# Performance work log

Hardware: AMD Instinct MI355X
Metric: run time of the kernel (lower is better)

## Reference

```python
import jax, jax.numpy as jnp
import numpy as np

N_NODES = 50000
N_EDGES = 1200000
IN_DIM = 256
OUT_DIM = 64
SLOPE = 0.2


def setup_inputs() -> dict:
    key = jax.random.key(0)
    k1, k2, k3, k4, k5 = jax.random.split(key, 5)
    h = jax.random.normal(k1, (N_NODES, IN_DIM), dtype=jnp.float32)
    # xavier_normal-ish scale for the linear weights
    W_fc = jax.random.normal(k2, (OUT_DIM, IN_DIM), dtype=jnp.float32) * (2.0 / (IN_DIM + OUT_DIM)) ** 0.5
    W_attn = jax.random.normal(k3, (1, 2 * OUT_DIM), dtype=jnp.float32) * (2.0 / (2 * OUT_DIM + 1)) ** 0.5
    src = jax.random.randint(k4, (N_EDGES,), 0, N_NODES, dtype=jnp.int32)
    dst = jax.random.randint(k5, (N_EDGES,), 0, N_NODES, dtype=jnp.int32)
    return {"h": h, "W_fc": W_fc, "W_attn": W_attn, "src": src, "dst": dst}


def reference(h, W_fc, W_attn, src, dst):
    # node transform: z = fc(h)                      [N, D]
    z = h @ W_fc.T
    # split attn weight so we never materialize the [E, 2D] concat
    a = W_attn[0]
    a_src, a_dst = a[:OUT_DIM], a[OUT_DIM:]
    s_src = z @ a_src            # [N]
    s_dst = z @ a_dst            # [N]
    # per-edge score: leaky_relu(attn_fc([z_src, z_dst]))
    e = jax.nn.leaky_relu(s_src[src] + s_dst[dst], negative_slope=SLOPE)  # [E]
    # edge softmax over incoming edges of each dst node
    m = jax.ops.segment_max(e, dst, num_segments=N_NODES)                 # [N]
    ex = jnp.exp(e - m[dst])                                              # [E]
    denom = jax.ops.segment_sum(ex, dst, num_segments=N_NODES)            # [N]
    alpha = ex / denom[dst]                                               # [E]
    # weighted scatter-sum of source features, then ELU
    agg = jax.ops.segment_sum(alpha[:, None] * z[src], dst, num_segments=N_NODES)  # [N, D]
    return jax.nn.elu(agg)
```

## Files before the change

### kernel.cpp

```cpp
#include <hip/hip_runtime.h>
#include <math.h>

#define N_NODES 50000
#define N_EDGES 1200000
#define IN_DIM  256
#define OUT_DIM 64
#define SLOPE   0.2f
#define BNODES  64
#define NBKT    782
#define NBKT_PAD 1024
#define EPB     1024
#define NCHUNK  1172
#define BCAP    2048
#define SSTRIDE 2240

typedef unsigned int   uint;
typedef unsigned short ushort;
typedef float  f32x4  __attribute__((ext_vector_type(4)));
typedef short  short8 __attribute__((ext_vector_type(8)));

__device__ inline ushort bf16_rne(float f) {
    uint u = __float_as_uint(f);
    u += 0x7FFF + ((u >> 16) & 1);
    return (ushort)(u >> 16);
}
__device__ inline float bf16_f32(ushort s) {
    return __uint_as_float(((uint)s) << 16);
}
__device__ inline ushort f32_f16(float f) {
    _Float16 h = (_Float16)f;
    return __builtin_bit_cast(ushort, h);
}
__device__ inline float f16_f32(ushort u) {
    return (float)__builtin_bit_cast(_Float16, u);
}

__global__ __launch_bounds__(256) void k_binprep(const int* __restrict__ src,
                                                 const int* __restrict__ dst,
                                                 const float* __restrict__ Wfc,
                                                 ushort* __restrict__ Whi,
                                                 ushort* __restrict__ Wlo,
                                                 uint* __restrict__ binned,
                                                 uint* __restrict__ tab) {
    if (blockIdx.x >= NCHUNK) {
        int i = (blockIdx.x - NCHUNK) * 256 + threadIdx.x;
        float f = Wfc[i];
        ushort hi = bf16_rne(f);
        Whi[i] = hi;
        Wlo[i] = bf16_rne(f - bf16_f32(hi));
        return;
    }
    __shared__ uint staged[EPB];
    __shared__ int lhist[NBKT_PAD];
    __shared__ int lcur[NBKT_PAD];
    __shared__ int ws[256];
    const int t = threadIdx.x;
    const int c = blockIdx.x;
    const int base = c * EPB;
    const int n = min(EPB, N_EDGES - base);

    ((int4*)lhist)[t] = int4{0, 0, 0, 0};
    __syncthreads();

    int4 d4, s4;
    bool act = (4 * t < n);
    if (act) {
        d4 = ((const int4*)(dst + base))[t];
        s4 = ((const int4*)(src + base))[t];
        atomicAdd(&lhist[d4.x >> 6], 1);
        atomicAdd(&lhist[d4.y >> 6], 1);
        atomicAdd(&lhist[d4.z >> 6], 1);
        atomicAdd(&lhist[d4.w >> 6], 1);
    }
    __syncthreads();

    int4 hv = ((const int4*)lhist)[t];
    int lsum = hv.x + hv.y + hv.z + hv.w;
    ws[t] = lsum; __syncthreads();
    #pragma unroll
    for (int off = 1; off < 256; off <<= 1) {
        int x = (t >= off) ? ws[t - off] : 0;
        __syncthreads(); ws[t] += x; __syncthreads();
    }
    int excl = ws[t] - lsum;
    int p0 = excl, p1 = p0 + hv.x, p2 = p1 + hv.y, p3 = p2 + hv.z;
    lcur[4 * t]     = p0;
    lcur[4 * t + 1] = p1;
    lcur[4 * t + 2] = p2;
    lcur[4 * t + 3] = p3;
    uint4 te;
    te.x = ((uint)p0 << 11) | (uint)hv.x;
    te.y = ((uint)p1 << 11) | (uint)hv.y;
    te.z = ((uint)p2 << 11) | (uint)hv.z;
    te.w = ((uint)p3 << 11) | (uint)hv.w;
    ((uint4*)(tab + (size_t)c * NBKT_PAD))[t] = te;
    __syncthreads();

    if (act) {
        int dd[4] = {d4.x, d4.y, d4.z, d4.w};
        int ss[4] = {s4.x, s4.y, s4.z, s4.w};
        #pragma unroll
        for (int u = 0; u < 4; ++u) {
            int b = dd[u] >> 6, dl = dd[u] & 63;
            int slot = atomicAdd(&lcur[b], 1);
            staged[slot] = ((uint)dl << 16) | (uint)ss[u];
        }
    }
    __syncthreads();
    #pragma unroll
    for (int k = 0; k < EPB / 256; ++k) {
        int i = k * 256 + t;
        if (i < n) binned[base + i] = staged[i];
    }
}

__global__ __launch_bounds__(64) void k_gemm(const float* __restrict__ h,
                                             const ushort* __restrict__ Whi,
                                             const ushort* __restrict__ Wlo,
                                             const float* __restrict__ Wattn,
                                             ushort* __restrict__ zh,
                                             float* __restrict__ sS,
                                             float* __restrict__ sD) {
    const int l   = threadIdx.x;
    const int r16 = l & 15;
    const int g   = l >> 4;
    const int base = blockIdx.x * 16;

    const float*  ha = h   + (size_t)(base + r16) * IN_DIM + g * 8;
    const ushort* wh = Whi + (size_t)r16 * IN_DIM + g * 8;
    const ushort* wl = Wlo + (size_t)r16 * IN_DIM + g * 8;

    f32x4 c[4] = {{0,0,0,0},{0,0,0,0},{0,0,0,0},{0,0,0,0}};

    #pragma unroll
    for (int ks = 0; ks < 8; ++ks) {
        float4 a0 = *(const float4*)(ha + ks * 32);
        float4 a1 = *(const float4*)(ha + ks * 32 + 4);
        float af[8] = {a0.x, a0.y, a0.z, a0.w, a1.x, a1.y, a1.z, a1.w};
        short8 ahi;
        #pragma unroll
        for (int i = 0; i < 8; ++i) ahi[i] = (short)bf16_rne(af[i]);
        #pragma unroll
        for (int n = 0; n < 4; ++n) {
            short8 bh = *(const short8*)(wh + n * 16 * IN_DIM + ks * 32);
            short8 bl = *(const short8*)(wl + n * 16 * IN_DIM + ks * 32);
            c[n] = __builtin_amdgcn_mfma_f32_16x16x32_bf16(ahi, bh, c[n], 0, 0, 0);
            c[n] = __builtin_amdgcn_mfma_f32_16x16x32_bf16(ahi, bl, c[n], 0, 0, 0);
        }
    }

    float aSv[4], aDv[4];
    #pragma unroll
    for (int n = 0; n < 4; ++n) {
        aSv[n] = Wattn[n * 16 + r16];
        aDv[n] = Wattn[OUT_DIM + n * 16 + r16];
    }
    #pragma unroll
    for (int r = 0; r < 4; ++r) {
        int node = base + g * 4 + r;
        float ss = 0.f, sd = 0.f;
        #pragma unroll
        for (int n = 0; n < 4; ++n) {
            float v = c[n][r];
            zh[(size_t)node * OUT_DIM + n * 16 + r16] = f32_f16(v);
            ss += v * aSv[n];
            sd += v * aDv[n];
        }
        ss += __shfl_xor(ss, 1); ss += __shfl_xor(ss, 2);
        ss += __shfl_xor(ss, 4); ss += __shfl_xor(ss, 8);
        sd += __shfl_xor(sd, 1); sd += __shfl_xor(sd, 2);
        sd += __shfl_xor(sd, 4); sd += __shfl_xor(sd, 8);
        if (r16 == 0) { sS[node] = ss; sD[node] = sd; }
    }
}

__global__ __launch_bounds__(256) void k_sort(const uint* __restrict__ binned,
                                              const uint* __restrict__ tab,
                                              const float* __restrict__ sS,
                                              const float* __restrict__ sD,
                                              uint* __restrict__ srcEx,
                                              int* __restrict__ rowptrFine,
                                              int* __restrict__ cntArr) {
    __shared__ uint lstage[BCAP];
    __shared__ uint lEdge[SSTRIDE];
    __shared__ int lhist[64], lcur[64], ws[256];
    __shared__ float ldsD[64];
    __shared__ int sPtot;
    const int b = blockIdx.x, t = threadIdx.x;
    const int node = (b << 6) + t;
    if (t < 64) {
        lhist[t] = 0;
        ldsD[t] = (node < N_NODES) ? sD[node] : 0.f;
    }
    __syncthreads();

    uint runs[5];
    int nck = 0, myCnt = 0;
    for (int c = t; c < NCHUNK; c += 256) {
        uint e = tab[(size_t)c * NBKT_PAD + b];
        runs[nck++] = e;
        myCnt += (int)(e & 0x7FF);
    }
    ws[t] = myCnt; __syncthreads();
    #pragma unroll
    for (int off = 1; off < 256; off <<= 1) {
        int x = (t >= off) ? ws[t - off] : 0;
        __syncthreads(); ws[t] += x; __syncthreads();
    }
    int pos = ws[t] - myCnt;
    int n = ws[255];
    __syncthreads();

    {
        int k = 0;
        for (int c = t; c < NCHUNK; c += 256, ++k) {
            uint e = runs[k];
            int cnt = (int)(e & 0x7FF);
            const uint* pB = binned + (size_t)c * EPB + (e >> 11);
            for (int i = 0; i < cnt; ++i) {
                uint w = pB[i];
                lstage[pos++] = w;
                atomicAdd(&lhist[w >> 16], 1);
            }
        }
    }
    __syncthreads();

    int pc = 0;
    if (t < 64) { pc = (lhist[t] + 3) & ~3; ws[t] = pc; }
    __syncthreads();
    #pragma unroll
    for (int off = 1; off < 64; off <<= 1) {
        int x = 0;
        if (t < 64 && t >= off) x = ws[t - off];
        __syncthreads();
        if (t < 64) ws[t] += x;
        __syncthreads();
    }
    if (t < 64) {
        int pexcl = ws[t] - pc;
        lcur[t] = pexcl;
        for (int j = lhist[t]; j < pc; ++j) lEdge[pexcl + j] = 0;
        if (node < N_NODES) {
            rowptrFine[node] = b * SSTRIDE + pexcl;
            cntArr[node] = pc;
        }
        if (t == 63) sPtot = ws[63];
    }
    __syncthreads();

    for (int i = t; i < n; i += 256) {
        uint w = lstage[i];
        int dl = (int)(w >> 16);
        int s  = (int)(w & 0xFFFF);
        float e = sS[s] + ldsD[dl];
        e = e > 0.f ? e : SLOPE * e;
        ushort exb = f32_f16(__expf(e));
        int slot = atomicAdd(&lcur[dl], 1);
        lEdge[slot] = ((w & 0xFFFFu) << 16) | (uint)exb;
    }
    __syncthreads();

    int ptot = sPtot;
    uint* dstp = srcEx + (size_t)b * SSTRIDE;
    for (int i = t; i < ptot; i += 256) dstp[i] = lEdge[i];
}

__global__ __launch_bounds__(256) void k_aggc(const uint2* __restrict__ zrow,
                                              const uint* __restrict__ srcEx,
                                              const int* __restrict__ rowptr,
                                              const int* __restrict__ cntArr,
                                              float* __restrict__ out) {
    int node = blockIdx.x * 4 + (threadIdx.x >> 6);
    int lane = threadIdx.x & 63;
    int q = lane >> 4, ql = lane & 15;
    int beg = rowptr[node];
    int cnt4 = cntArr[node];
    float a0 = 0.f, a1 = 0.f, a2 = 0.f, a3 = 0.f, den = 0.f;
    #pragma unroll 4
    for (int i = 0; i < cnt4; i += 4) {
        uint w = srcEx[beg + i + q];
        uint2 zp = zrow[((w >> 16) << 4) + ql];
        float ex = f16_f32((ushort)(w & 0xFFFF));
        a0 += ex * f16_f32((ushort)(zp.x & 0xFFFF));
        a1 += ex * f16_f32((ushort)(zp.x >> 16));
        a2 += ex * f16_f32((ushort)(zp.y & 0xFFFF));
        a3 += ex * f16_f32((ushort)(zp.y >> 16));
        den += ex;
    }
    a0 += __shfl_xor(a0, 16); a0 += __shfl_xor(a0, 32);
    a1 += __shfl_xor(a1, 16); a1 += __shfl_xor(a1, 32);
    a2 += __shfl_xor(a2, 16); a2 += __shfl_xor(a2, 32);
    a3 += __shfl_xor(a3, 16); a3 += __shfl_xor(a3, 32);
    den += __shfl_xor(den, 16); den += __shfl_xor(den, 32);
    if (q == 0) {
        float inv = den > 0.f ? 1.f / den : 0.f;
        float r0 = a0 * inv, r1 = a1 * inv, r2 = a2 * inv, r3 = a3 * inv;
        r0 = r0 > 0.f ? r0 : expm1f(r0);
        r1 = r1 > 0.f ? r1 : expm1f(r1);
        r2 = r2 > 0.f ? r2 : expm1f(r2);
        r3 = r3 > 0.f ? r3 : expm1f(r3);
        float4 r = make_float4(r0, r1, r2, r3);
        ((float4*)out)[(size_t)node * 16 + ql] = r;
    }
}

static inline char* alignup(char* p) {
    return (char*)(((uintptr_t)p + 63) & ~(uintptr_t)63);
}

extern "C" void kernel_launch(void* const* d_in, const int* in_sizes, int n_in,
                              void* d_out, int out_size, void* d_ws, size_t ws_size,
                              hipStream_t stream) {
    const float* h     = (const float*)d_in[0];
    const float* Wfc   = (const float*)d_in[1];
    const float* Wattn = (const float*)d_in[2];
    const int*   src   = (const int*)d_in[3];
    const int*   dst   = (const int*)d_in[4];
    float* out = (float*)d_out;

    char* p = (char*)d_ws;
    uint*   binned  = (uint*)p;   p = alignup(p + (size_t)N_EDGES * 4);
    uint*   tab     = (uint*)p;   p = alignup(p + (size_t)NCHUNK * NBKT_PAD * 4);
    uint*   srcEx   = (uint*)p;   p = alignup(p + (size_t)NBKT * SSTRIDE * 4);
    int*    rowptrF = (int*)p;    p = alignup(p + (size_t)N_NODES * 4);
    int*    cntArr  = (int*)p;    p = alignup(p + (size_t)N_NODES * 4);
    float*  sS      = (float*)p;  p = alignup(p + (size_t)N_NODES * 4);
    float*  sD      = (float*)p;  p = alignup(p + (size_t)N_NODES * 4);
    ushort* Whi     = (ushort*)p; p = alignup(p + OUT_DIM * IN_DIM * 2);
    ushort* Wlo     = (ushort*)p; p = alignup(p + OUT_DIM * IN_DIM * 2);
    ushort* zh      = (ushort*)p;

    k_binprep<<<NCHUNK + 64, 256, 0, stream>>>(src, dst, Wfc, Whi, Wlo, binned, tab);
    k_gemm<<<N_NODES / 16, 64, 0, stream>>>(h, Whi, Wlo, Wattn, zh, sS, sD);
    k_sort<<<NBKT, 256, 0, stream>>>(binned, tab, sS, sD, srcEx, rowptrF, cntArr);
    k_aggc<<<N_NODES / 4, 256, 0, stream>>>((const uint2*)zh, srcEx, rowptrF, cntArr, out);
}
```

Measured before the change: 93.47 us.

## Fuse sort and aggregation kernels; replace LDS block scans with wave shuffle scans

Merges the per-bucket sort kernel with the aggregation kernel so sorted edges stay in LDS and are consumed directly, removing the srcEx/rowptr/cnt global round trip and one launch. Block-wide prefix scans that used shared memory with many barriers become wavefront shuffle scans plus a small cross-wave combine. The cost is that aggregation now runs on only 782 blocks of 256 threads, each wave handling 16 nodes serially, so fewer waves are available to hide the latency of the random z gathers.

```diff
diff --git a/kernel.cpp b/kernel.cpp
--- a/kernel.cpp
+++ b/kernel.cpp
@@ -33,6 +33,14 @@
 }
 __device__ inline float f16_f32(ushort u) {
     return (float)__builtin_bit_cast(_Float16, u);
+}
+__device__ inline int waveInclScan(int v, int lane) {
+    #pragma unroll
+    for (int off = 1; off < 64; off <<= 1) {
+        int x = __shfl_up(v, off);
+        if (lane >= off) v += x;
+    }
+    return v;
 }
 
 __global__ __launch_bounds__(256) void k_binprep(const int* __restrict__ src,
@@ -53,8 +61,9 @@
     __shared__ uint staged[EPB];
     __shared__ int lhist[NBKT_PAD];
     __shared__ int lcur[NBKT_PAD];
-    __shared__ int ws[256];
+    __shared__ int wsums[4];
     const int t = threadIdx.x;
+    const int lane = t & 63, wid = t >> 6;
     const int c = blockIdx.x;
     const int base = c * EPB;
     const int n = min(EPB, N_EDGES - base);
@@ -76,13 +85,14 @@
 
     int4 hv = ((const int4*)lhist)[t];
     int lsum = hv.x + hv.y + hv.z + hv.w;
-    ws[t] = lsum; __syncthreads();
-    #pragma unroll
-    for (int off = 1; off < 256; off <<= 1) {
-        int x = (t >= off) ? ws[t - off] : 0;
-        __syncthreads(); ws[t] += x; __syncthreads();
-    }
-    int excl = ws[t] - lsum;
+    int incl = waveInclScan(lsum, lane);
+    if (lane == 63) wsums[wid] = incl;
+    __syncthreads();
+    int wbase = 0;
+    #pragma unroll
+    for (int w = 0; w < 4; ++w) if (w < wid) wbase += wsums[w];
+    int excl = wbase + incl - lsum;
+
     int p0 = excl, p1 = p0 + hv.x, p2 = p1 + hv.y, p3 = p2 + hv.z;
     lcur[4 * t]     = p0;
     lcur[4 * t + 1] = p1;
@@ -174,23 +184,24 @@
     }
 }
 
-__global__ __launch_bounds__(256) void k_sort(const uint* __restrict__ binned,
-                                              const uint* __restrict__ tab,
-                                              const float* __restrict__ sS,
-                                              const float* __restrict__ sD,
-                                              uint* __restrict__ srcEx,
-                                              int* __restrict__ rowptrFine,
-                                              int* __restrict__ cntArr) {
+__global__ __launch_bounds__(256) void k_sortagg(const uint* __restrict__ binned,
+                                                 const uint* __restrict__ tab,
+                                                 const float* __restrict__ sS,
+                                                 const float* __restrict__ sD,
+                                                 const uint2* __restrict__ zrow,
+                                                 float* __restrict__ out) {
     __shared__ uint lstage[BCAP];
     __shared__ uint lEdge[SSTRIDE];
-    __shared__ int lhist[64], lcur[64], ws[256];
+    __shared__ int lhist[64], lcur[64], lpbeg[64], lpc[64];
     __shared__ float ldsD[64];
-    __shared__ int sPtot;
+    __shared__ int wsums[4];
     const int b = blockIdx.x, t = threadIdx.x;
-    const int node = (b << 6) + t;
+    const int lane = t & 63, wid = t >> 6;
+    const int node0 = b << 6;
     if (t < 64) {
         lhist[t] = 0;
-        ldsD[t] = (node < N_NODES) ? sD[node] : 0.f;
+        int nd = node0 + t;
+        ldsD[t] = (nd < N_NODES) ? sD[nd] : 0.f;
     }
     __syncthreads();
 
@@ -201,15 +212,16 @@
         runs[nck++] = e;
         myCnt += (int)(e & 0x7FF);
     }
-    ws[t] = myCnt; __syncthreads();
-    #pragma unroll
-    for (int off = 1; off < 256; off <<= 1) {
-        int x = (t >= off) ? ws[t - off] : 0;
-        __syncthreads(); ws[t] += x; __syncthreads();
-    }
-    int pos = ws[t] - myCnt;
-    int n = ws[255];
-    __syncthreads();
+    int incl = waveInclScan(myCnt, lane);
+    if (lane == 63) wsums[wid] = incl;
+    __syncthreads();
+    int wbase = 0;
+    #pragma unroll
+    for (int w = 0; w < 4; ++w) if (w < wid) wbase += wsums[w];
+    int pos = wbase + incl - myCnt;
+    int n = 0;
+    #pragma unroll
+    for (int w = 0; w < 4; ++w) n += wsums[w];
 
     {
         int k = 0;
@@ -226,26 +238,15 @@
     }
     __syncthreads();
 
-    int pc = 0;
-    if (t < 64) { pc = (lhist[t] + 3) & ~3; ws[t] = pc; }
-    __syncthreads();
-    #pragma unroll
-    for (int off = 1; off < 64; off <<= 1) {
-        int x = 0;
-        if (t < 64 && t >= off) x = ws[t - off];
-        __syncthreads();
-        if (t < 64) ws[t] += x;
-        __syncthreads();
-    }
     if (t < 64) {
-        int pexcl = ws[t] - pc;
+        int hc = lhist[t];
+        int pc = (hc + 3) & ~3;
+        int pincl = waveInclScan(pc, t);
+        int pexcl = pincl - pc;
+        lpbeg[t] = pexcl;
         lcur[t] = pexcl;
-        for (int j = lhist[t]; j < pc; ++j) lEdge[pexcl + j] = 0;
-        if (node < N_NODES) {
-            rowptrFine[node] = b * SSTRIDE + pexcl;
-            cntArr[node] = pc;
-        }
-        if (t == 63) sPtot = ws[63];
+        lpc[t] = pc;
+        for (int j = hc; j < pc; ++j) lEdge[pexcl + j] = 0;
     }
     __syncthreads();
 
@@ -261,47 +262,40 @@
     }
     __syncthreads();
 
-    int ptot = sPtot;
-    uint* dstp = srcEx + (size_t)b * SSTRIDE;
-    for (int i = t; i < ptot; i += 256) dstp[i] = lEdge[i];
-}
-
-__global__ __launch_bounds__(256) void k_aggc(const uint2* __restrict__ zrow,
-                                              const uint* __restrict__ srcEx,
-                                              const int* __restrict__ rowptr,
-                                              const int* __restrict__ cntArr,
-                                              float* __restrict__ out) {
-    int node = blockIdx.x * 4 + (threadIdx.x >> 6);
-    int lane = threadIdx.x & 63;
-    int q = lane >> 4, ql = lane & 15;
-    int beg = rowptr[node];
-    int cnt4 = cntArr[node];
-    float a0 = 0.f, a1 = 0.f, a2 = 0.f, a3 = 0.f, den = 0.f;
-    #pragma unroll 4
-    for (int i = 0; i < cnt4; i += 4) {
-        uint w = srcEx[beg + i + q];
-        uint2 zp = zrow[((w >> 16) << 4) + ql];
-        float ex = f16_f32((ushort)(w & 0xFFFF));
-        a0 += ex * f16_f32((ushort)(zp.x & 0xFFFF));
-        a1 += ex * f16_f32((ushort)(zp.x >> 16));
-        a2 += ex * f16_f32((ushort)(zp.y & 0xFFFF));
-        a3 += ex * f16_f32((ushort)(zp.y >> 16));
-        den += ex;
-    }
-    a0 += __shfl_xor(a0, 16); a0 += __shfl_xor(a0, 32);
-    a1 += __shfl_xor(a1, 16); a1 += __shfl_xor(a1, 32);
-    a2 += __shfl_xor(a2, 16); a2 += __shfl_xor(a2, 32);
-    a3 += __shfl_xor(a3, 16); a3 += __shfl_xor(a3, 32);
-    den += __shfl_xor(den, 16); den += __shfl_xor(den, 32);
-    if (q == 0) {
-        float inv = den > 0.f ? 1.f / den : 0.f;
-        float r0 = a0 * inv, r1 = a1 * inv, r2 = a2 * inv, r3 = a3 * inv;
-        r0 = r0 > 0.f ? r0 : expm1f(r0);
-        r1 = r1 > 0.f ? r1 : expm1f(r1);
-        r2 = r2 > 0.f ? r2 : expm1f(r2);
-        r3 = r3 > 0.f ? r3 : expm1f(r3);
-        float4 r = make_float4(r0, r1, r2, r3);
-        ((float4*)out)[(size_t)node * 16 + ql] = r;
+    const int q = lane >> 4, ql = lane & 15;
+    #pragma unroll 1
+    for (int nl0 = 0; nl0 < 16; ++nl0) {
+        int nl = wid * 16 + nl0;
+        int beg = lpbeg[nl];
+        int cnt4 = lpc[nl];
+        float a0 = 0.f, a1 = 0.f, a2 = 0.f, a3 = 0.f, den = 0.f;
+        #pragma unroll 4
+        for (int i = 0; i < cnt4; i += 4) {
+            uint w = lEdge[beg + i + q];
+            uint2 zp = zrow[((w >> 16) << 4) + ql];
+            float ex = f16_f32((ushort)(w & 0xFFFF));
+            a0 += ex * f16_f32((ushort)(zp.x & 0xFFFF));
+            a1 += ex * f16_f32((ushort)(zp.x >> 16));
+            a2 += ex * f16_f32((ushort)(zp.y & 0xFFFF));
+            a3 += ex * f16_f32((ushort)(zp.y >> 16));
+            den += ex;
+        }
+        a0 += __shfl_xor(a0, 16); a0 += __shfl_xor(a0, 32);
+        a1 += __shfl_xor(a1, 16); a1 += __shfl_xor(a1, 32);
+        a2 += __shfl_xor(a2, 16); a2 += __shfl_xor(a2, 32);
+        a3 += __shfl_xor(a3, 16); a3 += __shfl_xor(a3, 32);
+        den += __shfl_xor(den, 16); den += __shfl_xor(den, 32);
+        int node = node0 + nl;
+        if (q == 0 && node < N_NODES) {
+            float inv = den > 0.f ? 1.f / den : 0.f;
+            float r0 = a0 * inv, r1 = a1 * inv, r2 = a2 * inv, r3 = a3 * inv;
+            r0 = r0 > 0.f ? r0 : expm1f(r0);
+            r1 = r1 > 0.f ? r1 : expm1f(r1);
+            r2 = r2 > 0.f ? r2 : expm1f(r2);
+            r3 = r3 > 0.f ? r3 : expm1f(r3);
+            float4 r = make_float4(r0, r1, r2, r3);
+            ((float4*)out)[(size_t)node * 16 + ql] = r;
+        }
     }
 }
 
@@ -322,9 +316,6 @@
     char* p = (char*)d_ws;
     uint*   binned  = (uint*)p;   p = alignup(p + (size_t)N_EDGES * 4);
     uint*   tab     = (uint*)p;   p = alignup(p + (size_t)NCHUNK * NBKT_PAD * 4);
-    uint*   srcEx   = (uint*)p;   p = alignup(p + (size_t)NBKT * SSTRIDE * 4);
-    int*    rowptrF = (int*)p;    p = alignup(p + (size_t)N_NODES * 4);
-    int*    cntArr  = (int*)p;    p = alignup(p + (size_t)N_NODES * 4);
     float*  sS      = (float*)p;  p = alignup(p + (size_t)N_NODES * 4);
     float*  sD      = (float*)p;  p = alignup(p + (size_t)N_NODES * 4);
     ushort* Whi     = (ushort*)p; p = alignup(p + OUT_DIM * IN_DIM * 2);
@@ -333,6 +324,5 @@
 
     k_binprep<<<NCHUNK + 64, 256, 0, stream>>>(src, dst, Wfc, Whi, Wlo, binned, tab);
     k_gemm<<<N_NODES / 16, 64, 0, stream>>>(h, Whi, Wlo, Wattn, zh, sS, sD);
-    k_sort<<<NBKT, 256, 0, stream>>>(binned, tab, sS, sD, srcEx, rowptrF, cntArr);
-    k_aggc<<<N_NODES / 4, 256, 0, stream>>>((const uint2*)zh, srcEx, rowptrF, cntArr, out);
-}
+    k_sortagg<<<NBKT, 256, 0, stream>>>(binned, tab, sS, sD, (const uint2*)zh, out);
+}
```

After: 93.75 us. No clear change (+0.3%).
